# Performance work log

Hardware: AMD Instinct MI355X
Metric: run time of the kernel (lower is better)

## Reference

```python
import jax, jax.numpy as jnp
import numpy as np

DIM = 1024
DEPTH = 8
DIM_HEAD = 64
HEADS = 16
NUM_Q = 16
EMB = 768
OUT = 1024
FF_INNER = 4 * DIM
INNER = DIM_HEAD * HEADS  # 1024
B, N1 = 64, 577
EPS = 1e-5


def _ln(x, g, b):
    mu = jnp.mean(x, axis=-1, keepdims=True)
    var = jnp.mean((x - mu) ** 2, axis=-1, keepdims=True)
    return (x - mu) * jax.lax.rsqrt(var + EPS) * g + b


def setup_inputs() -> dict:
    key = jax.random.key(0)
    ks = jax.random.split(key, 16)
    std = 0.02
    inp = {
        'x': jax.random.normal(ks[0], (B, N1, EMB), jnp.float32),
        'queries': jax.random.normal(ks[1], (1, NUM_Q, DIM), jnp.float32) / DIM ** 0.5,
        'proj_in_w': jax.random.normal(ks[2], (EMB, DIM), jnp.float32) * std,
        'proj_in_b': jnp.zeros((DIM,), jnp.float32),
        'ln1_g': jnp.ones((DEPTH, DIM), jnp.float32),
        'ln1_b': jnp.zeros((DEPTH, DIM), jnp.float32),
        'ln2_g': jnp.ones((DEPTH, DIM), jnp.float32),
        'ln2_b': jnp.zeros((DEPTH, DIM), jnp.float32),
        'wq': jax.random.normal(ks[3], (DEPTH, DIM, INNER), jnp.float32) * std,
        'wkv': jax.random.normal(ks[4], (DEPTH, DIM, 2 * INNER), jnp.float32) * std,
        'wo': jax.random.normal(ks[5], (DEPTH, INNER, DIM), jnp.float32) * std,
        'ffln_g': jnp.ones((DEPTH, DIM), jnp.float32),
        'ffln_b': jnp.zeros((DEPTH, DIM), jnp.float32),
        'w1': jax.random.normal(ks[6], (DEPTH, DIM, FF_INNER), jnp.float32) * std,
        'w2': jax.random.normal(ks[7], (DEPTH, FF_INNER, DIM), jnp.float32) * std,
        'proj_out_w': jax.random.normal(ks[8], (DIM, OUT), jnp.float32) * std,
        'proj_out_b': jnp.zeros((OUT,), jnp.float32),
        'nout_g': jnp.ones((OUT,), jnp.float32),
        'nout_b': jnp.zeros((OUT,), jnp.float32),
    }
    return inp


def reference(x, queries, proj_in_w, proj_in_b, ln1_g, ln1_b, ln2_g, ln2_b,
              wq, wkv, wo, ffln_g, ffln_b, w1, w2,
              proj_out_w, proj_out_b, nout_g, nout_b):
    b = x.shape[0]
    xp = x @ proj_in_w + proj_in_b          # (b, n1, dim)
    latents0 = jnp.broadcast_to(queries, (b, NUM_Q, DIM))
    scale = DIM_HEAD ** -0.25               # applied to both q and k

    def layer(latents, p):
        (g1, b1, g2, b2, Wq, Wkv, Wo, gf, bf, W1, W2) = p
        xn = _ln(xp, g1, b1)                # (b, n1, dim)
        lt = _ln(latents, g2, b2)           # (b, nq, dim)
        q = lt @ Wq                         # (b, nq, inner)
        kv_in = jnp.concatenate([xn, lt], axis=1)   # (b, n1+nq, dim)
        kv = kv_in @ Wkv                    # (b, n1+nq, 2*inner)
        k, v = jnp.split(kv, 2, axis=-1)
        L = kv_in.shape[1]
        qh = q.reshape(b, NUM_Q, HEADS, DIM_HEAD).transpose(0, 2, 1, 3)
        kh = k.reshape(b, L, HEADS, DIM_HEAD).transpose(0, 2, 1, 3)
        vh = v.reshape(b, L, HEADS, DIM_HEAD).transpose(0, 2, 1, 3)
        logits = jnp.einsum('bhqd,bhkd->bhqk', qh * scale, kh * scale)
        w = jax.nn.softmax(logits.astype(jnp.float32), axis=-1).astype(logits.dtype)
        o = jnp.einsum('bhqk,bhkd->bhqd', w, vh)
        o = o.transpose(0, 2, 1, 3).reshape(b, NUM_Q, INNER) @ Wo
        latents = o + latents
        h = _ln(latents, gf, bf) @ W1
        h = jax.nn.gelu(h, approximate=False)
        latents = h @ W2 + latents
        return latents, None

    params = (ln1_g, ln1_b, ln2_g, ln2_b, wq, wkv, wo, ffln_g, ffln_b, w1, w2)
    latents, _ = jax.lax.scan(layer, latents0, params)
    out = latents @ proj_out_w + proj_out_b
    return _ln(out, nout_g, nout_b)
```

## Files before the change

kernel.cpp:

```cpp
#include <hip/hip_runtime.h>
#include <hip/hip_bf16.h>
#include <math.h>

#define DEV __device__ __forceinline__

typedef __bf16 bf16x8 __attribute__((ext_vector_type(8)));
typedef float f32x4 __attribute__((ext_vector_type(4)));
typedef unsigned short u16x8 __attribute__((ext_vector_type(8)));
typedef unsigned short u16x4 __attribute__((ext_vector_type(4)));

DEV float b2f(unsigned short u){ unsigned int i = ((unsigned int)u)<<16; float f; __builtin_memcpy(&f,&i,4); return f; }
DEV unsigned short f2b(float x){ unsigned int i; __builtin_memcpy(&i,&x,4); unsigned int r = i + 0x7FFFu + ((i>>16)&1u); return (unsigned short)(r>>16); }

DEV int swz(int row, int elem){ return row*64 + ((((elem>>3) ^ row) & 7)<<3) + (elem&7); }

enum { EPI_F32=0, EPI_GELU=2, EPI_RESF32=3 };

template<int BM, int BN>
__global__ __launch_bounds__(256)
void gemm2(const unsigned short* __restrict__ A, const unsigned short* __restrict__ Bt,
           const float* __restrict__ bias, unsigned short* __restrict__ Out,
           int M, int N, int K, int NT)
{
    constexpr int MR = BM/32, NR = BN/32;
    constexpr int LA = BM/32, LB = BN/32;
    __shared__ unsigned short As[BM*64];
    __shared__ unsigned short Bs[BN*64];
    const int tid  = threadIdx.x;
    const int lane = tid & 63;
    const int wave = tid >> 6;
    const int wr = wave >> 1, wc = wave & 1;
    const int chunk = gridDim.x >> 3;
    const int nb = (blockIdx.x & 7)*chunk + (blockIdx.x >> 3);
    const int nt = nb % NT, mt = nb / NT;

    f32x4 acc[MR][NR];
    #pragma unroll
    for (int m=0;m<MR;m++)
      #pragma unroll
      for (int n=0;n<NR;n++) acc[m][n] = f32x4{0.f,0.f,0.f,0.f};

    const unsigned short* pA[LA]; const unsigned short* pB[LB];
    int dA[LA], dB[LB];
    #pragma unroll
    for (int i=0;i<LA;i++){
      int e = (i*256+tid)*8; int row = e>>6, col = e&63;
      int gr = mt*BM + row; if (gr > M-1) gr = M-1;
      pA[i] = A + (size_t)gr*K + col;
      dA[i] = swz(row,col);
    }
    #pragma unroll
    for (int i=0;i<LB;i++){
      int e = (i*256+tid)*8; int row = e>>6, col = e&63;
      pB[i] = Bt + (size_t)(nt*BN+row)*K + col;
      dB[i] = swz(row,col);
    }

    u16x8 rA0[LA], rB0[LB], rA1[LA], rB1[LB];
    auto issue0 = [&](int k0){
      #pragma unroll
      for (int i=0;i<LA;i++) rA0[i] = *reinterpret_cast<const u16x8*>(pA[i]+k0);
      #pragma unroll
      for (int i=0;i<LB;i++) rB0[i] = *reinterpret_cast<const u16x8*>(pB[i]+k0);
    };
    auto issue1 = [&](int k0){
      #pragma unroll
      for (int i=0;i<LA;i++) rA1[i] = *reinterpret_cast<const u16x8*>(pA[i]+k0);
      #pragma unroll
      for (int i=0;i<LB;i++) rB1[i] = *reinterpret_cast<const u16x8*>(pB[i]+k0);
    };
    auto commit0 = [&](){
      #pragma unroll
      for (int i=0;i<LA;i++) *reinterpret_cast<u16x8*>(&As[dA[i]]) = rA0[i];
      #pragma unroll
      for (int i=0;i<LB;i++) *reinterpret_cast<u16x8*>(&Bs[dB[i]]) = rB0[i];
    };
    auto commit1 = [&](){
      #pragma unroll
      for (int i=0;i<LA;i++) *reinterpret_cast<u16x8*>(&As[dA[i]]) = rA1[i];
      #pragma unroll
      for (int i=0;i<LB;i++) *reinterpret_cast<u16x8*>(&Bs[dB[i]]) = rB1[i];
    };
    auto compute = [&](){
      #pragma unroll
      for (int kk=0; kk<2; kk++){
        bf16x8 av[MR], bv[NR];
        #pragma unroll
        for (int m=0;m<MR;m++){
          int r = wr*(BM/2) + m*16 + (lane&15);
          av[m] = (bf16x8)(*reinterpret_cast<const u16x8*>(&As[swz(r, kk*32 + (lane>>4)*8)]));
        }
        #pragma unroll
        for (int n=0;n<NR;n++){
          int r = wc*(BN/2) + n*16 + (lane&15);
          bv[n] = (bf16x8)(*reinterpret_cast<const u16x8*>(&Bs[swz(r, kk*32 + (lane>>4)*8)]));
        }
        #pragma unroll
        for (int m=0;m<MR;m++)
          #pragma unroll
          for (int n=0;n<NR;n++)
            acc[m][n] = __builtin_amdgcn_mfma_f32_16x16x32_bf16(av[m], bv[n], acc[m][n], 0, 0, 0);
      }
    };

    const int nk = K / 64;
    issue0(0); issue1(64);
    #pragma unroll 1
    for (int kt=0; kt<nk; kt+=2){
      __syncthreads();
      commit0();
      __syncthreads();
      if (kt+2 < nk) issue0((kt+2)*64);
      compute();
      __syncthreads();
      commit1();
      __syncthreads();
      if (kt+3 < nk) issue1((kt+3)*64);
      compute();
    }

    #pragma unroll
    for (int m=0;m<MR;m++){
      #pragma unroll
      for (int n=0;n<NR;n++){
        #pragma unroll
        for (int r=0;r<4;r++){
          int row = mt*BM + wr*(BM/2) + m*16 + (lane>>4)*4 + r;
          int col = nt*BN + wc*(BN/2) + n*16 + (lane&15);
          if (row < M){
            float v = acc[m][n][r];
            if (bias) v += bias[col];
            Out[(size_t)row*N + col] = f2b(v);
          }
        }
      }
    }
}

template<int EPI>
__global__ __launch_bounds__(256)
void gemm_sp2(const unsigned short* __restrict__ AH, const unsigned short* __restrict__ AL,
              const unsigned short* __restrict__ BH, const unsigned short* __restrict__ BL,
              const float* __restrict__ bias, const float* __restrict__ Res,
              void* __restrict__ Out, unsigned short* __restrict__ OutL,
              int M, int N, int K, int NT)
{
    constexpr int MR=2, NR=2;
    __shared__ unsigned short As[2*64*64];
    __shared__ unsigned short Bs[2*64*64];
    const int tid  = threadIdx.x;
    const int lane = tid & 63;
    const int wave = tid >> 6;
    const int wr = wave >> 1, wc = wave & 1;
    const int chunk = gridDim.x >> 3;
    const int nb = (blockIdx.x & 7)*chunk + (blockIdx.x >> 3);
    const int nt = nb % NT, mt = nb / NT;

    f32x4 acc[MR][NR];
    #pragma unroll
    for (int m=0;m<MR;m++)
      #pragma unroll
      for (int n=0;n<NR;n++) acc[m][n] = f32x4{0.f,0.f,0.f,0.f};

    const unsigned short *pA[2], *pB[2];
    int dst[2];
    #pragma unroll
    for (int i=0;i<2;i++){
      int e = (i*256+tid)*8; int row = e>>6, col = e&63;
      pA[i] = AH + (size_t)(mt*64+row)*K + col;
      pB[i] = BH + (size_t)(nt*64+row)*K + col;
      dst[i] = swz(row,col);
    }
    const size_t dAL = (size_t)(AL - AH);
    const size_t dBL = (size_t)(BL - BH);

    u16x8 rAH0[2], rAL0[2], rBH0[2], rBL0[2];
    u16x8 rAH1[2], rAL1[2], rBH1[2], rBL1[2];
    auto issue0 = [&](int k0){
      #pragma unroll
      for (int i=0;i<2;i++){
        rAH0[i] = *reinterpret_cast<const u16x8*>(pA[i]+k0);
        rAL0[i] = *reinterpret_cast<const u16x8*>(pA[i]+dAL+k0);
        rBH0[i] = *reinterpret_cast<const u16x8*>(pB[i]+k0);
        rBL0[i] = *reinterpret_cast<const u16x8*>(pB[i]+dBL+k0);
      }
    };
    auto issue1 = [&](int k0){
      #pragma unroll
      for (int i=0;i<2;i++){
        rAH1[i] = *reinterpret_cast<const u16x8*>(pA[i]+k0);
        rAL1[i] = *reinterpret_cast<const u16x8*>(pA[i]+dAL+k0);
        rBH1[i] = *reinterpret_cast<const u16x8*>(pB[i]+k0);
        rBL1[i] = *reinterpret_cast<const u16x8*>(pB[i]+dBL+k0);
      }
    };
    auto commit0 = [&](){
      #pragma unroll
      for (int i=0;i<2;i++){
        *reinterpret_cast<u16x8*>(&As[dst[i]])      = rAH0[i];
        *reinterpret_cast<u16x8*>(&As[4096+dst[i]]) = rAL0[i];
        *reinterpret_cast<u16x8*>(&Bs[dst[i]])      = rBH0[i];
        *reinterpret_cast<u16x8*>(&Bs[4096+dst[i]]) = rBL0[i];
      }
    };
    auto commit1 = [&](){
      #pragma unroll
      for (int i=0;i<2;i++){
        *reinterpret_cast<u16x8*>(&As[dst[i]])      = rAH1[i];
        *reinterpret_cast<u16x8*>(&As[4096+dst[i]]) = rAL1[i];
        *reinterpret_cast<u16x8*>(&Bs[dst[i]])      = rBH1[i];
        *reinterpret_cast<u16x8*>(&Bs[4096+dst[i]]) = rBL1[i];
      }
    };
    auto compute = [&](){
      #pragma unroll
      for (int kk=0; kk<2; kk++){
        bf16x8 ah[MR], al[MR], bh[NR], bl[NR];
        #pragma unroll
        for (int m=0;m<MR;m++){
          int a = swz(wr*32 + m*16 + (lane&15), kk*32 + (lane>>4)*8);
          ah[m] = (bf16x8)(*reinterpret_cast<const u16x8*>(&As[a]));
          al[m] = (bf16x8)(*reinterpret_cast<const u16x8*>(&As[4096 + a]));
        }
        #pragma unroll
        for (int n=0;n<NR;n++){
          int a = swz(wc*32 + n*16 + (lane&15), kk*32 + (lane>>4)*8);
          bh[n] = (bf16x8)(*reinterpret_cast<const u16x8*>(&Bs[a]));
          bl[n] = (bf16x8)(*reinterpret_cast<const u16x8*>(&Bs[4096 + a]));
        }
        #pragma unroll
        for (int m=0;m<MR;m++)
          #pragma unroll
          for (int n=0;n<NR;n++){
            acc[m][n] = __builtin_amdgcn_mfma_f32_16x16x32_bf16(ah[m], bh[n], acc[m][n], 0, 0, 0);
            acc[m][n] = __builtin_amdgcn_mfma_f32_16x16x32_bf16(ah[m], bl[n], acc[m][n], 0, 0, 0);
            acc[m][n] = __builtin_amdgcn_mfma_f32_16x16x32_bf16(al[m], bh[n], acc[m][n], 0, 0, 0);
          }
      }
    };

    const int nk = K / 64;
    issue0(0); issue1(64);
    #pragma unroll 1
    for (int kt=0; kt<nk; kt+=2){
      __syncthreads();
      commit0();
      __syncthreads();
      if (kt+2 < nk) issue0((kt+2)*64);
      compute();
      __syncthreads();
      commit1();
      __syncthreads();
      if (kt+3 < nk) issue1((kt+3)*64);
      compute();
    }

    #pragma unroll
    for (int m=0;m<MR;m++){
      #pragma unroll
      for (int n=0;n<NR;n++){
        #pragma unroll
        for (int r=0;r<4;r++){
          int row = mt*64 + wr*32 + m*16 + (lane>>4)*4 + r;
          int col = nt*64 + wc*32 + n*16 + (lane&15);
          float v = acc[m][n][r];
          if (bias) v += bias[col];
          if constexpr (EPI==EPI_GELU){
            v = 0.5f*v*(1.0f + erff(v*0.70710678118654752f));
            unsigned short hi = f2b(v);
            ((unsigned short*)Out)[(size_t)row*N + col] = hi;
            OutL[(size_t)row*N + col] = f2b(v - b2f(hi));
          } else {
            if constexpr (EPI==EPI_RESF32) v += Res[(size_t)row*N + col];
            ((float*)Out)[(size_t)row*N + col] = v;
          }
        }
      }
    }
}

enum { OM_F32=0, OM_BF16=1, OM_SPLIT=2 };
template<bool INF32, int OM, bool HASGB>
__global__ __launch_bounds__(256)
void ln_rows(const void* __restrict__ In, void* __restrict__ Out,
             unsigned short* __restrict__ OutL,
             const float* __restrict__ g, const float* __restrict__ bb)
{
  const int row = blockIdx.x;
  const int tid = threadIdx.x;
  const size_t base = (size_t)row*1024 + tid*4;
  float v[4];
  if constexpr (INF32){
    f32x4 t = *reinterpret_cast<const f32x4*>((const float*)In + base);
    v[0]=t[0]; v[1]=t[1]; v[2]=t[2]; v[3]=t[3];
  } else {
    u16x4 t = *reinterpret_cast<const u16x4*>((const unsigned short*)In + base);
    #pragma unroll
    for (int j=0;j<4;j++) v[j] = b2f(t[j]);
  }
  float s = v[0]+v[1]+v[2]+v[3];
  float q = v[0]*v[0]+v[1]*v[1]+v[2]*v[2]+v[3]*v[3];
  #pragma unroll
  for (int o=32;o>0;o>>=1){ s += __shfl_xor(s,o,64); q += __shfl_xor(q,o,64); }
  __shared__ float sm[8];
  const int wave = tid>>6, lane = tid&63;
  if (lane==0){ sm[wave] = s; sm[4+wave] = q; }
  __syncthreads();
  s = sm[0]+sm[1]+sm[2]+sm[3];
  q = sm[4]+sm[5]+sm[6]+sm[7];
  const float mean = s*(1.f/1024.f);
  const float rstd = rsqrtf(fmaxf(q*(1.f/1024.f) - mean*mean, 0.f) + 1e-5f);
  #pragma unroll
  for (int j=0;j<4;j++){
    float t2 = (v[j]-mean)*rstd;
    if constexpr (HASGB) t2 = t2*g[tid*4+j] + bb[tid*4+j];
    v[j] = t2;
  }
  if constexpr (OM==OM_F32){
    f32x4 t{v[0],v[1],v[2],v[3]};
    *reinterpret_cast<f32x4*>((float*)Out + base) = t;
  } else if constexpr (OM==OM_BF16){
    u16x4 t{f2b(v[0]),f2b(v[1]),f2b(v[2]),f2b(v[3])};
    *reinterpret_cast<u16x4*>((unsigned short*)Out + base) = t;
  } else {
    u16x4 h{f2b(v[0]),f2b(v[1]),f2b(v[2]),f2b(v[3])};
    u16x4 l{f2b(v[0]-b2f(h[0])),f2b(v[1]-b2f(h[1])),f2b(v[2]-b2f(h[2])),f2b(v[3]-b2f(h[3]))};
    *reinterpret_cast<u16x4*>((unsigned short*)Out + base) = h;
    *reinterpret_cast<u16x4*>(OutL + base) = l;
  }
}

template<bool LO>
__global__ __launch_bounds__(256)
void transpose_cvt_b(const float* __restrict__ W, const float* __restrict__ rs,
                     unsigned short* __restrict__ Wt, unsigned short* __restrict__ Wtlo,
                     int K, int N, size_t wLS, size_t tLS, int dstRowOff)
{
  const int l = blockIdx.z;
  const float* Wl = W + (size_t)l*wLS;
  __shared__ float t[32][33];
  const int tx = threadIdx.x & 31, ty = threadIdx.x >> 5;
  const int n0 = blockIdx.x*32, k0 = blockIdx.y*32;
  #pragma unroll
  for (int j=0;j<4;j++){
    int r = ty + j*8;
    float w = Wl[(size_t)(k0+r)*N + n0 + tx];
    if (rs) w *= rs[l*1024 + k0+r];
    t[r][tx] = w;
  }
  __syncthreads();
  #pragma unroll
  for (int j=0;j<4;j++){
    int r = ty + j*8;
    float w = t[tx][r];
    unsigned short hi = f2b(w);
    size_t di = (size_t)l*tLS + (size_t)(dstRowOff + n0 + r)*K + k0 + tx;
    Wt[di] = hi;
    if constexpr (LO) Wtlo[di] = f2b(w - b2f(hi));
  }
}

__global__ __launch_bounds__(256)
void biaskv_kernel(const float* __restrict__ ln1b, const float* __restrict__ wkv,
                   float* __restrict__ out)
{
  const int l = blockIdx.y;
  const int n = blockIdx.x*256 + threadIdx.x;
  const float* b1 = ln1b + l*1024;
  const float* W  = wkv + (size_t)l*1024*2048;
  float s = 0.f;
  for (int k=0;k<1024;k++) s += b1[k]*W[(size_t)k*2048 + n];
  out[l*2048 + n] = s;
}

__global__ __launch_bounds__(256)
void init_latents(const float* __restrict__ Q, float* __restrict__ L)
{
  size_t idx = ((size_t)blockIdx.x*256 + threadIdx.x)*4;
  int row = (int)(idx >> 10);
  int col = (int)(idx & 1023);
  f32x4 t = *reinterpret_cast<const f32x4*>(Q + (size_t)(row & 15)*1024 + col);
  *reinterpret_cast<f32x4*>(L + idx) = t;
}

__global__ __launch_bounds__(256)
void cvt_f32_bf16(const float* __restrict__ In, unsigned short* __restrict__ Out, size_t n4)
{
  size_t i = (size_t)blockIdx.x*256 + threadIdx.x;
  if (i >= n4) return;
  f32x4 t = *reinterpret_cast<const f32x4*>(In + i*4);
  u16x4 u{f2b(t[0]),f2b(t[1]),f2b(t[2]),f2b(t[3])};
  *reinterpret_cast<u16x4*>(Out + i*4) = u;
}

__global__ __launch_bounds__(256)
void cvt_f32b_pair(const float* __restrict__ In, unsigned short* __restrict__ Oh,
                   unsigned short* __restrict__ Ol)
{
  size_t idx = ((size_t)blockIdx.x*256 + threadIdx.x)*4;
  f32x4 t = *reinterpret_cast<const f32x4*>(In + idx);
  u16x4 h{f2b(t[0]),f2b(t[1]),f2b(t[2]),f2b(t[3])};
  u16x4 l{f2b(t[0]-b2f(h[0])),f2b(t[1]-b2f(h[1])),f2b(t[2]-b2f(h[2])),f2b(t[3]-b2f(h[3]))};
  *reinterpret_cast<u16x4*>(Oh + idx) = h;
  *reinterpret_cast<u16x4*>(Ol + idx) = l;
}

__global__ __launch_bounds__(256)
void attn_kernel(const float* __restrict__ QKVf,
                 const unsigned short* __restrict__ KVX,
                 unsigned short* __restrict__ ATTOh,
                 unsigned short* __restrict__ ATTOl)
{
  __shared__ float qs[16][64];
  __shared__ float ws[16][600];
  const int tid = threadIdx.x;
  const int bh = blockIdx.x;
  const int b = bh >> 4, h = bh & 15;

  {
    int idx = tid*4;
    int qi = idx >> 6, d = idx & 63;
    f32x4 t = *reinterpret_cast<const f32x4*>(QKVf + (size_t)(b*16+qi)*3072 + h*64 + d);
    #pragma unroll
    for (int j=0;j<4;j++) qs[qi][d+j] = 0.125f * t[j];
  }
  __syncthreads();

  for (int r = tid; r < 593; r += 256){
    float a[16];
    #pragma unroll
    for (int qi=0;qi<16;qi++) a[qi] = 0.f;
    if (r < 577){
      const unsigned short* krow = KVX + ((size_t)(b*577 + r)*2048 + h*64);
      #pragma unroll 4
      for (int d4=0; d4<16; d4++){
        u16x4 k4 = *reinterpret_cast<const u16x4*>(krow + d4*4);
        float kf0=b2f(k4[0]), kf1=b2f(k4[1]), kf2=b2f(k4[2]), kf3=b2f(k4[3]);
        #pragma unroll
        for (int qi=0;qi<16;qi++){
          f32x4 q4 = *reinterpret_cast<const f32x4*>(&qs[qi][d4*4]);
          a[qi] += q4[0]*kf0 + q4[1]*kf1 + q4[2]*kf2 + q4[3]*kf3;
        }
      }
    } else {
      const float* krow = QKVf + (size_t)(b*16 + (r-577))*3072 + 1024 + h*64;
      #pragma unroll 4
      for (int d4=0; d4<16; d4++){
        f32x4 k4 = *reinterpret_cast<const f32x4*>(krow + d4*4);
        #pragma unroll
        for (int qi=0;qi<16;qi++){
          f32x4 q4 = *reinterpret_cast<const f32x4*>(&qs[qi][d4*4]);
          a[qi] += q4[0]*k4[0] + q4[1]*k4[1] + q4[2]*k4[2] + q4[3]*k4[3];
        }
      }
    }
    #pragma unroll
    for (int qi=0;qi<16;qi++) ws[qi][r] = a[qi];
  }
  __syncthreads();

  const int wave = tid>>6, lane = tid&63;
  for (int qi = wave; qi < 16; qi += 4){
    float m = -1e30f;
    for (int r = lane; r < 593; r += 64) m = fmaxf(m, ws[qi][r]);
    #pragma unroll
    for (int o=32;o>0;o>>=1) m = fmaxf(m, __shfl_xor(m,o,64));
    float s = 0.f;
    for (int r = lane; r < 593; r += 64){ float e = expf(ws[qi][r]-m); ws[qi][r] = e; s += e; }
    #pragma unroll
    for (int o=32;o>0;o>>=1) s += __shfl_xor(s,o,64);
    float inv = 1.f/s;
    for (int r = lane; r < 593; r += 64) ws[qi][r] *= inv;
  }
  __syncthreads();

  const int d = tid & 63, qg = tid >> 6;
  float o0=0.f,o1=0.f,o2=0.f,o3=0.f;
  for (int rr=0; rr<576; rr+=4){
    f32x4 w0 = *reinterpret_cast<const f32x4*>(&ws[qg   ][rr]);
    f32x4 w1 = *reinterpret_cast<const f32x4*>(&ws[qg+4 ][rr]);
    f32x4 w2 = *reinterpret_cast<const f32x4*>(&ws[qg+8 ][rr]);
    f32x4 w3 = *reinterpret_cast<const f32x4*>(&ws[qg+12][rr]);
    #pragma unroll
    for (int j=0;j<4;j++){
      const unsigned short* vrow = KVX + ((size_t)(b*577 + rr + j)*2048 + 1024 + h*64);
      float v = b2f(vrow[d]);
      o0 += w0[j]*v; o1 += w1[j]*v; o2 += w2[j]*v; o3 += w3[j]*v;
    }
  }
  {
    float v = b2f(KVX[(size_t)(b*577 + 576)*2048 + 1024 + h*64 + d]);
    o0 += ws[qg][576]*v; o1 += ws[qg+4][576]*v; o2 += ws[qg+8][576]*v; o3 += ws[qg+12][576]*v;
  }
  for (int r=577; r<593; r++){
    float v = QKVf[(size_t)(b*16 + (r-577))*3072 + 2048 + h*64 + d];
    o0 += ws[qg][r]*v; o1 += ws[qg+4][r]*v; o2 += ws[qg+8][r]*v; o3 += ws[qg+12][r]*v;
  }
  float ov[4] = {o0,o1,o2,o3};
  #pragma unroll
  for (int j=0;j<4;j++){
    size_t idx = (size_t)(b*16+qg+4*j)*1024 + h*64 + d;
    unsigned short hi = f2b(ov[j]);
    ATTOh[idx] = hi;
    ATTOl[idx] = f2b(ov[j] - b2f(hi));
  }
}

extern "C" void kernel_launch(void* const* d_in, const int* in_sizes, int n_in,
                              void* d_out, int out_size, void* d_ws, size_t ws_size,
                              hipStream_t stream)
{
  const float* x    = (const float*)d_in[0];
  const float* qry  = (const float*)d_in[1];
  const float* piw  = (const float*)d_in[2];
  const float* pib  = (const float*)d_in[3];
  const float* ln1g = (const float*)d_in[4];
  const float* ln1b = (const float*)d_in[5];
  const float* ln2g = (const float*)d_in[6];
  const float* ln2b = (const float*)d_in[7];
  const float* wq   = (const float*)d_in[8];
  const float* wkv  = (const float*)d_in[9];
  const float* wo   = (const float*)d_in[10];
  const float* ffg  = (const float*)d_in[11];
  const float* ffb  = (const float*)d_in[12];
  const float* w1   = (const float*)d_in[13];
  const float* w2   = (const float*)d_in[14];
  const float* pow_ = (const float*)d_in[15];
  const float* pob  = (const float*)d_in[16];
  const float* ng   = (const float*)d_in[17];
  const float* nb   = (const float*)d_in[18];

  const int MROWS = 64*577;
  char* wsb = (char*)d_ws;
  size_t off = 0;
  auto alloc = [&](size_t bytes)->char*{
    char* p = wsb + off; off = (off + bytes + 255) & ~(size_t)255; return p;
  };
  unsigned short* XB     = (unsigned short*)alloc((size_t)36992*768*2);
  unsigned short* XP     = (unsigned short*)alloc((size_t)36992*1024*2);
  unsigned short* KVX    = (unsigned short*)alloc((size_t)36992*2048*2);
  unsigned short* WpiT   = (unsigned short*)alloc((size_t)1024*768*2);
  unsigned short* WkvTs  = (unsigned short*)alloc((size_t)8*2048*1024*2);
  unsigned short* WqkvT  = (unsigned short*)alloc((size_t)8*3072*1024*2);
  unsigned short* WqkvTl = (unsigned short*)alloc((size_t)8*3072*1024*2);
  unsigned short* WoT    = (unsigned short*)alloc((size_t)8*1024*1024*2);
  unsigned short* WoTl   = (unsigned short*)alloc((size_t)8*1024*1024*2);
  unsigned short* W1T    = (unsigned short*)alloc((size_t)4096*1024*2);
  unsigned short* W1Tl   = (unsigned short*)alloc((size_t)4096*1024*2);
  unsigned short* W2T    = (unsigned short*)alloc((size_t)1024*4096*2);
  unsigned short* W2Tl   = (unsigned short*)alloc((size_t)1024*4096*2);
  float*          BKV    = (float*)alloc((size_t)8*2048*4);
  unsigned short* LTh    = (unsigned short*)alloc((size_t)1024*1024*2);
  unsigned short* LTl    = (unsigned short*)alloc((size_t)1024*1024*2);
  float*          QKVf   = (float*)alloc((size_t)1024*3072*4);
  unsigned short* ATTOh  = (unsigned short*)alloc((size_t)1024*1024*2);
  unsigned short* ATTOl  = (unsigned short*)alloc((size_t)1024*1024*2);
  unsigned short* FFHh   = (unsigned short*)alloc((size_t)1024*4096*2);
  unsigned short* FFHl   = (unsigned short*)alloc((size_t)1024*4096*2);
  unsigned short* LATBh  = (unsigned short*)alloc((size_t)1024*1024*2);
  unsigned short* LATBl  = (unsigned short*)alloc((size_t)1024*1024*2);
  float*          LATF   = (float*)alloc((size_t)1024*1024*4);
  if (off > ws_size) return;

  dim3 blk(256);

  cvt_f32_bf16<<<dim3((36928*768/4 + 255)/256), blk, 0, stream>>>(x, XB, (size_t)36928*768/4);
  transpose_cvt_b<false><<<dim3(32,24,1), blk, 0, stream>>>(piw, nullptr, WpiT, nullptr, 768, 1024, 0, 0, 0);
  transpose_cvt_b<false><<<dim3(64,32,8), blk, 0, stream>>>(wkv, ln1g, WkvTs, nullptr, 1024, 2048, (size_t)1024*2048, (size_t)2048*1024, 0);
  transpose_cvt_b<true ><<<dim3(32,32,8), blk, 0, stream>>>(wq,  nullptr, WqkvT, WqkvTl, 1024, 1024, (size_t)1024*1024, (size_t)3072*1024, 0);
  transpose_cvt_b<true ><<<dim3(64,32,8), blk, 0, stream>>>(wkv, nullptr, WqkvT, WqkvTl, 1024, 2048, (size_t)1024*2048, (size_t)3072*1024, 1024);
  transpose_cvt_b<true ><<<dim3(32,32,8), blk, 0, stream>>>(wo,  nullptr, WoT, WoTl, 1024, 1024, (size_t)1024*1024, (size_t)1024*1024, 0);
  biaskv_kernel<<<dim3(8,8), blk, 0, stream>>>(ln1b, wkv, BKV);
  init_latents<<<dim3(1024), blk, 0, stream>>>(qry, LATF);

  gemm2<128,128><<<dim3(8*289), blk, 0, stream>>>(XB, WpiT, pib, XP, MROWS, 1024, 768, 8);
  ln_rows<false,OM_BF16,false><<<dim3(MROWS), blk, 0, stream>>>(XP, XP, nullptr, nullptr, nullptr);

  for (int l=0; l<8; l++){
    transpose_cvt_b<true><<<dim3(128,32,1), blk, 0, stream>>>(w1 + (size_t)l*1024*4096, nullptr, W1T, W1Tl, 1024, 4096, 0, 0, 0);
    transpose_cvt_b<true><<<dim3(32,128,1), blk, 0, stream>>>(w2 + (size_t)l*4096*1024, nullptr, W2T, W2Tl, 4096, 1024, 0, 0, 0);

    ln_rows<true,OM_SPLIT,true><<<dim3(1024), blk, 0, stream>>>(LATF, LTh, LTl, ln2g + l*1024, ln2b + l*1024);
    gemm_sp2<EPI_F32><<<dim3(16*48), blk, 0, stream>>>(
        LTh, LTl, WqkvT + (size_t)l*3072*1024, WqkvTl + (size_t)l*3072*1024,
        nullptr, nullptr, QKVf, nullptr, 1024, 3072, 1024, 48);
    gemm2<128,128><<<dim3(16*289), blk, 0, stream>>>(
        XP, WkvTs + (size_t)l*2048*1024, BKV + l*2048, KVX, MROWS, 2048, 1024, 16);
    attn_kernel<<<dim3(1024), blk, 0, stream>>>(QKVf, KVX, ATTOh, ATTOl);
    gemm_sp2<EPI_RESF32><<<dim3(16*16), blk, 0, stream>>>(
        ATTOh, ATTOl, WoT + (size_t)l*1024*1024, WoTl + (size_t)l*1024*1024,
        nullptr, LATF, LATF, nullptr, 1024, 1024, 1024, 16);
    ln_rows<true,OM_SPLIT,true><<<dim3(1024), blk, 0, stream>>>(LATF, LTh, LTl, ffg + l*1024, ffb + l*1024);
    gemm_sp2<EPI_GELU><<<dim3(16*64), blk, 0, stream>>>(
        LTh, LTl, W1T, W1Tl, nullptr, nullptr, FFHh, FFHl, 1024, 4096, 1024, 64);
    gemm_sp2<EPI_RESF32><<<dim3(16*16), blk, 0, stream>>>(
        FFHh, FFHl, W2T, W2Tl, nullptr, LATF, LATF, nullptr, 1024, 1024, 4096, 16);
  }

  transpose_cvt_b<true><<<dim3(32,32,1), blk, 0, stream>>>(pow_, nullptr, W1T, W1Tl, 1024, 1024, 0, 0, 0);
  cvt_f32b_pair<<<dim3(1024), blk, 0, stream>>>(LATF, LATBh, LATBl);
  gemm_sp2<EPI_F32><<<dim3(16*16), blk, 0, stream>>>(
      LATBh, LATBl, W1T, W1Tl, pob, nullptr, QKVf, nullptr, 1024, 1024, 1024, 16);
  ln_rows<true,OM_F32,true><<<dim3(1024), blk, 0, stream>>>(QKVf, d_out, nullptr, ng, nb);
}
```

Baseline: 5.335 ms.

## Replace 128x128 bf16 GEMM with 256x256-tile 512-thread GEMM for projections

The large projection GEMMs (input projection and per-layer KV over 36928 rows) now use a new kernel with 256x256 output tiles, 8 waves per block, and 8x4 MFMA accumulators per wave. This doubles arithmetic intensity per tile and cuts global/LDS traffic per FLOP. The double register-buffered prefetch is reduced to a single buffer, and the XCD-aware block index remapping is dropped. Risks are high register pressure (128 accumulator floats per lane), lower occupancy, a 64KB LDS footprint, and less prefetch overlap.

```diff
diff --git a/kernel.cpp b/kernel.cpp
--- a/kernel.cpp
+++ b/kernel.cpp
@@ -16,117 +16,87 @@
 
 enum { EPI_F32=0, EPI_GELU=2, EPI_RESF32=3 };
 
-template<int BM, int BN>
-__global__ __launch_bounds__(256)
-void gemm2(const unsigned short* __restrict__ A, const unsigned short* __restrict__ Bt,
+__global__ __launch_bounds__(512)
+void gemm3(const unsigned short* __restrict__ A, const unsigned short* __restrict__ Bt,
            const float* __restrict__ bias, unsigned short* __restrict__ Out,
            int M, int N, int K, int NT)
 {
-    constexpr int MR = BM/32, NR = BN/32;
-    constexpr int LA = BM/32, LB = BN/32;
-    __shared__ unsigned short As[BM*64];
-    __shared__ unsigned short Bs[BN*64];
+    __shared__ unsigned short As[256*64];
+    __shared__ unsigned short Bs[256*64];
     const int tid  = threadIdx.x;
     const int lane = tid & 63;
     const int wave = tid >> 6;
-    const int wr = wave >> 1, wc = wave & 1;
-    const int chunk = gridDim.x >> 3;
-    const int nb = (blockIdx.x & 7)*chunk + (blockIdx.x >> 3);
+    const int wr = wave >> 2, wc = wave & 3;
+    const int nb = blockIdx.x;
     const int nt = nb % NT, mt = nb / NT;
 
-    f32x4 acc[MR][NR];
-    #pragma unroll
-    for (int m=0;m<MR;m++)
-      #pragma unroll
-      for (int n=0;n<NR;n++) acc[m][n] = f32x4{0.f,0.f,0.f,0.f};
-
-    const unsigned short* pA[LA]; const unsigned short* pB[LB];
-    int dA[LA], dB[LB];
-    #pragma unroll
-    for (int i=0;i<LA;i++){
-      int e = (i*256+tid)*8; int row = e>>6, col = e&63;
-      int gr = mt*BM + row; if (gr > M-1) gr = M-1;
+    f32x4 acc[8][4];
+    #pragma unroll
+    for (int m=0;m<8;m++)
+      #pragma unroll
+      for (int n=0;n<4;n++) acc[m][n] = f32x4{0.f,0.f,0.f,0.f};
+
+    const unsigned short* pA[4]; const unsigned short* pB[4];
+    int dA[4], dB[4];
+    #pragma unroll
+    for (int i=0;i<4;i++){
+      int e = (i*512+tid)*8; int row = e>>6, col = e&63;
+      int gr = mt*256 + row; if (gr > M-1) gr = M-1;
       pA[i] = A + (size_t)gr*K + col;
       dA[i] = swz(row,col);
-    }
-    #pragma unroll
-    for (int i=0;i<LB;i++){
-      int e = (i*256+tid)*8; int row = e>>6, col = e&63;
-      pB[i] = Bt + (size_t)(nt*BN+row)*K + col;
+      pB[i] = Bt + (size_t)(nt*256+row)*K + col;
       dB[i] = swz(row,col);
     }
 
-    u16x8 rA0[LA], rB0[LB], rA1[LA], rB1[LB];
-    auto issue0 = [&](int k0){
-      #pragma unroll
-      for (int i=0;i<LA;i++) rA0[i] = *reinterpret_cast<const u16x8*>(pA[i]+k0);
-      #pragma unroll
-      for (int i=0;i<LB;i++) rB0[i] = *reinterpret_cast<const u16x8*>(pB[i]+k0);
-    };
-    auto issue1 = [&](int k0){
-      #pragma unroll
-      for (int i=0;i<LA;i++) rA1[i] = *reinterpret_cast<const u16x8*>(pA[i]+k0);
-      #pragma unroll
-      for (int i=0;i<LB;i++) rB1[i] = *reinterpret_cast<const u16x8*>(pB[i]+k0);
-    };
-    auto commit0 = [&](){
-      #pragma unroll
-      for (int i=0;i<LA;i++) *reinterpret_cast<u16x8*>(&As[dA[i]]) = rA0[i];
-      #pragma unroll
-      for (int i=0;i<LB;i++) *reinterpret_cast<u16x8*>(&Bs[dB[i]]) = rB0[i];
-    };
-    auto commit1 = [&](){
-      #pragma unroll
-      for (int i=0;i<LA;i++) *reinterpret_cast<u16x8*>(&As[dA[i]]) = rA1[i];
-      #pragma unroll
-      for (int i=0;i<LB;i++) *reinterpret_cast<u16x8*>(&Bs[dB[i]]) = rB1[i];
-    };
-    auto compute = [&](){
+    u16x8 rA[4], rB[4];
+    auto issue = [&](int k0){
+      #pragma unroll
+      for (int i=0;i<4;i++) rA[i] = *reinterpret_cast<const u16x8*>(pA[i]+k0);
+      #pragma unroll
+      for (int i=0;i<4;i++) rB[i] = *reinterpret_cast<const u16x8*>(pB[i]+k0);
+    };
+    auto commit = [&](){
+      #pragma unroll
+      for (int i=0;i<4;i++) *reinterpret_cast<u16x8*>(&As[dA[i]]) = rA[i];
+      #pragma unroll
+      for (int i=0;i<4;i++) *reinterpret_cast<u16x8*>(&Bs[dB[i]]) = rB[i];
+    };
+
+    issue(0);
+    const int nk = K / 64;
+    #pragma unroll 1
+    for (int kt=0; kt<nk; kt++){
+      __syncthreads();
+      commit();
+      __syncthreads();
+      if (kt+1 < nk) issue((kt+1)*64);
       #pragma unroll
       for (int kk=0; kk<2; kk++){
-        bf16x8 av[MR], bv[NR];
-        #pragma unroll
-        for (int m=0;m<MR;m++){
-          int r = wr*(BM/2) + m*16 + (lane&15);
-          av[m] = (bf16x8)(*reinterpret_cast<const u16x8*>(&As[swz(r, kk*32 + (lane>>4)*8)]));
-        }
-        #pragma unroll
-        for (int n=0;n<NR;n++){
-          int r = wc*(BN/2) + n*16 + (lane&15);
+        bf16x8 bv[4];
+        #pragma unroll
+        for (int n=0;n<4;n++){
+          int r = wc*64 + n*16 + (lane&15);
           bv[n] = (bf16x8)(*reinterpret_cast<const u16x8*>(&Bs[swz(r, kk*32 + (lane>>4)*8)]));
         }
         #pragma unroll
-        for (int m=0;m<MR;m++)
+        for (int m=0;m<8;m++){
+          int r = wr*128 + m*16 + (lane&15);
+          bf16x8 av = (bf16x8)(*reinterpret_cast<const u16x8*>(&As[swz(r, kk*32 + (lane>>4)*8)]));
           #pragma unroll
-          for (int n=0;n<NR;n++)
-            acc[m][n] = __builtin_amdgcn_mfma_f32_16x16x32_bf16(av[m], bv[n], acc[m][n], 0, 0, 0);
-      }
-    };
-
-    const int nk = K / 64;
-    issue0(0); issue1(64);
-    #pragma unroll 1
-    for (int kt=0; kt<nk; kt+=2){
-      __syncthreads();
-      commit0();
-      __syncthreads();
-      if (kt+2 < nk) issue0((kt+2)*64);
-      compute();
-      __syncthreads();
-      commit1();
-      __syncthreads();
-      if (kt+3 < nk) issue1((kt+3)*64);
-      compute();
-    }
-
-    #pragma unroll
-    for (int m=0;m<MR;m++){
-      #pragma unroll
-      for (int n=0;n<NR;n++){
+          for (int n=0;n<4;n++)
+            acc[m][n] = __builtin_amdgcn_mfma_f32_16x16x32_bf16(av, bv[n], acc[m][n], 0, 0, 0);
+        }
+      }
+    }
+
+    #pragma unroll
+    for (int m=0;m<8;m++){
+      #pragma unroll
+      for (int n=0;n<4;n++){
         #pragma unroll
         for (int r=0;r<4;r++){
-          int row = mt*BM + wr*(BM/2) + m*16 + (lane>>4)*4 + r;
-          int col = nt*BN + wc*(BN/2) + n*16 + (lane&15);
+          int row = mt*256 + wr*128 + m*16 + (lane>>4)*4 + r;
+          int col = nt*256 + wc*64 + n*16 + (lane&15);
           if (row < M){
             float v = acc[m][n][r];
             if (bias) v += bias[col];
@@ -563,6 +533,7 @@
   if (off > ws_size) return;
 
   dim3 blk(256);
+  dim3 blk5(512);
 
   cvt_f32_bf16<<<dim3((36928*768/4 + 255)/256), blk, 0, stream>>>(x, XB, (size_t)36928*768/4);
   transpose_cvt_b<false><<<dim3(32,24,1), blk, 0, stream>>>(piw, nullptr, WpiT, nullptr, 768, 1024, 0, 0, 0);
@@ -573,7 +544,7 @@
   biaskv_kernel<<<dim3(8,8), blk, 0, stream>>>(ln1b, wkv, BKV);
   init_latents<<<dim3(1024), blk, 0, stream>>>(qry, LATF);
 
-  gemm2<128,128><<<dim3(8*289), blk, 0, stream>>>(XB, WpiT, pib, XP, MROWS, 1024, 768, 8);
+  gemm3<<<dim3(145*4), blk5, 0, stream>>>(XB, WpiT, pib, XP, MROWS, 1024, 768, 4);
   ln_rows<false,OM_BF16,false><<<dim3(MROWS), blk, 0, stream>>>(XP, XP, nullptr, nullptr, nullptr);
 
   for (int l=0; l<8; l++){
@@ -584,8 +555,8 @@
     gemm_sp2<EPI_F32><<<dim3(16*48), blk, 0, stream>>>(
         LTh, LTl, WqkvT + (size_t)l*3072*1024, WqkvTl + (size_t)l*3072*1024,
         nullptr, nullptr, QKVf, nullptr, 1024, 3072, 1024, 48);
-    gemm2<128,128><<<dim3(16*289), blk, 0, stream>>>(
-        XP, WkvTs + (size_t)l*2048*1024, BKV + l*2048, KVX, MROWS, 2048, 1024, 16);
+    gemm3<<<dim3(145*8), blk5, 0, stream>>>(
+        XP, WkvTs + (size_t)l*2048*1024, BKV + l*2048, KVX, MROWS, 2048, 1024, 8);
     attn_kernel<<<dim3(1024), blk, 0, stream>>>(QKVf, KVX, ATTOh, ATTOl);
     gemm_sp2<EPI_RESF32><<<dim3(16*16), blk, 0, stream>>>(
         ATTOh, ATTOl, WoT + (size_t)l*1024*1024, WoTl + (size_t)l*1024*1024,
```

Measured after the change: 5.084 ms. 4.7% less time.
